# Kernel tuning notes

Hardware: AMD Instinct MI355X
Metric: run time of the kernel (lower is better)

Reference implementation:

```python
import jax, jax.numpy as jnp
import numpy as np

J_THR = 0.5
E_THR = 0.5
STRIDE = 4.0
N_LAYERS = 3
NFEAT = 256
SCORER_HIDDEN = 128


def setup_inputs() -> dict:
    key = jax.random.key(0)
    ks = jax.random.split(key, 8)
    B, C, h, w = 4, NFEAT, 128, 128
    inp = {
        "j_logits": jax.random.normal(ks[0], (B, 1, h, w), dtype=jnp.float32),
        "offsets": jax.random.uniform(ks[1], (B, 2, h, w), dtype=jnp.float32),
        "node_feats_map": jax.random.normal(ks[2], (B, C, h, w), dtype=jnp.float32) * 0.1,
        "W_self": jax.random.normal(ks[3], (N_LAYERS, C, C), dtype=jnp.float32) / np.sqrt(C).astype(np.float32),
        "W_nbr": jax.random.normal(ks[4], (N_LAYERS, C, C), dtype=jnp.float32) / np.sqrt(C).astype(np.float32),
        "b_gnn": jnp.zeros((N_LAYERS, C), dtype=jnp.float32),
        "Ws1": jax.random.normal(ks[5], (2 * C, SCORER_HIDDEN), dtype=jnp.float32) / np.sqrt(2.0 * C).astype(np.float32),
        "bs1": jnp.zeros((SCORER_HIDDEN,), dtype=jnp.float32),
        "Ws2": jax.random.normal(ks[6], (SCORER_HIDDEN,), dtype=jnp.float32) / np.sqrt(SCORER_HIDDEN).astype(np.float32),
        "bs2": jnp.zeros((), dtype=jnp.float32),
        "max_nodes": 256,
    }
    return inp


def _complete_graph(n):
    # src repeats node i (n-1) times; dst enumerates all j != i, matching torch complete_graph
    src = np.repeat(np.arange(n), n - 1)
    grid = np.tile(np.arange(n), (n, 1))
    dst = grid[~np.eye(n, dtype=bool)]
    return jnp.asarray(src, dtype=jnp.int32), jnp.asarray(dst, dtype=jnp.int32)


def reference(j_logits, offsets, node_feats_map, W_self, W_nbr, b_gnn, Ws1, bs1, Ws2, bs2, max_nodes):
    B, _, h, w = j_logits.shape
    C = node_feats_map.shape[1]
    N = int(max_nodes)
    src, dst = _complete_graph(N)  # [E], E = N*(N-1)

    def per_image(jl, off, nmap):
        prob = jax.nn.sigmoid(jl[0].reshape(-1))            # [h*w]
        topv, topi = jax.lax.top_k(prob, N)                  # fixed-size stream compaction
        valid = topv > J_THR                                 # [N] mask replacing dynamic nonzero
        iy = topi // w
        ix = topi % w
        yo = off[0].reshape(-1)[topi]
        xo = off[1].reshape(-1)[topi]
        xs = (ix.astype(jnp.float32) + 0.5 + xo) * STRIDE
        ys = (iy.astype(jnp.float32) + 0.5 + yo) * STRIDE
        nodes = jnp.stack([xs, ys], axis=-1)                 # [N,2]
        x = nmap.reshape(C, -1)[:, topi].T * valid[:, None].astype(nmap.dtype)  # [N,C]
        ev = (valid[src] & valid[dst]).astype(x.dtype)       # [E] edge validity
        deg = jax.ops.segment_sum(ev, dst, num_segments=N)   # [N]
        inv_deg = jnp.where(deg > 0, 1.0 / jnp.maximum(deg, 1.0), 0.0)
        for l in range(W_self.shape[0]):
            msg = x[src] * ev[:, None]                       # gather + mask [E,C]
            agg = jax.ops.segment_sum(msg, dst, num_segments=N) * inv_deg[:, None]
            x = jax.nn.relu(x @ W_self[l] + agg @ W_nbr[l] + b_gnn[l]) * valid[:, None].astype(x.dtype)
        hcat = jnp.concatenate([x[src], x[dst]], axis=-1)    # [E,2C]
        hid = jax.nn.relu(hcat @ Ws1 + bs1)                  # [E,H]
        logits = hid @ Ws2 + bs2                             # [E]
        probs = jax.nn.sigmoid(logits)
        keep = (probs > E_THR) & (ev > 0)
        return nodes, x, logits, keep

    nodes, node_emb, edge_logits, keep = jax.vmap(per_image)(j_logits, offsets, node_feats_map)
    return nodes, node_emb, edge_logits, keep
```

## Files before the change

kernel.cpp:

```cpp
#include <hip/hip_runtime.h>

#define NPIX 16384
#define NN   256
#define CC   256
#define HH   128
#define EE   65280
#define BB   4
#define NG   16

typedef __attribute__((ext_vector_type(8))) short short8;
typedef __attribute__((ext_vector_type(4))) float f32x4;

__device__ __forceinline__ unsigned short f2bf(float f){
  unsigned b = __float_as_uint(f);
  return (unsigned short)((b + 0x7fffu + ((b >> 16) & 1u)) >> 16);
}
__device__ __forceinline__ float bf2f(unsigned short s){ return __uint_as_float(((unsigned)s) << 16); }

__global__ __launch_bounds__(1024) void k_topk(
    const float* __restrict__ jl, const float* __restrict__ off,
    int* __restrict__ topi, int* __restrict__ valid, float* __restrict__ inv_deg,
    float* __restrict__ out_nodes, float* __restrict__ Sbuf,
    const float* __restrict__ Wself, const float* __restrict__ Wnbr,
    const float* __restrict__ Ws1,
    unsigned short* __restrict__ wbfT, unsigned short* __restrict__ wuvT)
{
  __shared__ int hist[NG][257];
  __shared__ int histT[256];
  __shared__ unsigned long long s_sel[NN];
  __shared__ unsigned long long s_T;
  __shared__ int s_digit, s_krem, s_cnt, s_vcnt, s_break;
  __shared__ float tile[32][33];

  const int bid = blockIdx.x;
  const int tid = threadIdx.x;

  if (bid >= BB) {
    const int blk = bid - BB;
    const int m = blk >> 6;
    const int t = blk & 63;
    const int r  = tid >> 5;
    const int cl = tid & 31;
    if (m < 6) {
      const int tr = t >> 3, tc = t & 7;
      const float* src = (m < 3) ? (Wself + (size_t)m*65536) : (Wnbr + (size_t)(m-3)*65536);
      tile[r][cl] = src[(size_t)(tr*32 + r)*256 + tc*32 + cl];
      __syncthreads();
      wbfT[(size_t)m*65536 + (size_t)(tc*32 + r)*256 + tr*32 + cl] = f2bf(tile[cl][r]);
    } else {
      const int tr = t >> 2, tc = t & 3;
      tile[r][cl] = Ws1[(size_t)(tr*32 + r)*128 + tc*32 + cl];
      __syncthreads();
      int h  = tc*32 + r;
      int cgx = tr*32 + cl;
      int col = h + ((cgx >= 256) ? 128 : 0);
      wuvT[(size_t)col*256 + (cgx & 255)] = f2bf(tile[cl][r]);
    }
    return;
  }

  const int b = bid;
  const int grp = tid >> 6;
  if (tid == 0) { s_cnt = 0; s_vcnt = 0; }

  {
    int l = tid >> 8, c = tid & 255;
    Sbuf[l*BB*CC + b*CC + c] = 0.0f;
  }

  unsigned long long rk[16];
  const float* p = jl + (size_t)b * NPIX;
  #pragma unroll
  for (int r = 0; r < 16; ++r) {
    int i = tid + (r << 10);
    float x = p[i];
    float pr = 1.0f / (1.0f + expf(-x));
    unsigned bits = __float_as_uint(pr);
    rk[r] = ((unsigned long long)bits << 32) | (unsigned)(0xFFFFFFFFu - (unsigned)i);
  }

  unsigned long long prefix = 0;
  int k = NN;
  int shift = 56;
  int brk = 0;
  for (int pass = 0; pass < 8 && !brk; ++pass) {
    shift = 56 - 8 * pass;
    for (int i = tid; i < NG * 257; i += 1024) ((int*)hist)[i] = 0;
    __syncthreads();
    unsigned long long pmask = (pass == 0) ? 0ULL : (~0ULL << (shift + 8));
    #pragma unroll
    for (int r = 0; r < 16; ++r) {
      unsigned long long kk = rk[r];
      if ((kk & pmask) == prefix)
        atomicAdd(&hist[grp][(int)((kk >> shift) & 255)], 1);
    }
    __syncthreads();
    if (tid < 256) {
      int t = 0;
      #pragma unroll
      for (int g = 0; g < NG; ++g) t += hist[g][tid];
      histT[tid] = t;
    }
    __syncthreads();
    if (tid < 64) {
      int h0 = histT[4*tid + 0], h1 = histT[4*tid + 1];
      int h2 = histT[4*tid + 2], h3 = histT[4*tid + 3];
      int tot = h0 + h1 + h2 + h3;
      int suf = tot;
      #pragma unroll
      for (int d = 1; d < 64; d <<= 1) {
        int o = __shfl_down(suf, d);
        if (tid + d < 64) suf += o;
      }
      int above = suf - tot;
      int c3 = h3 + above;
      int c2 = c3 + h2;
      int c1 = c2 + h1;
      int c0 = c1 + h0;
      if      (c3 >= k && above < k) { s_digit = 4*tid+3; s_krem = k - above; s_break = (h3 == 1); }
      else if (c2 >= k && c3    < k) { s_digit = 4*tid+2; s_krem = k - c3;    s_break = (h2 == 1); }
      else if (c1 >= k && c2    < k) { s_digit = 4*tid+1; s_krem = k - c2;    s_break = (h1 == 1); }
      else if (c0 >= k && c1    < k) { s_digit = 4*tid+0; s_krem = k - c1;    s_break = (h0 == 1); }
    }
    __syncthreads();
    prefix |= ((unsigned long long)s_digit) << shift;
    k = s_krem;
    brk = s_break;
  }

  if (shift == 0) {
    if (tid == 0) s_T = prefix;
  } else {
    unsigned long long known_mask = ~0ULL << shift;
    #pragma unroll
    for (int r = 0; r < 16; ++r)
      if ((rk[r] & known_mask) == prefix) s_T = rk[r];
  }
  __syncthreads();
  unsigned long long T = s_T;

  #pragma unroll
  for (int r = 0; r < 16; ++r) {
    unsigned long long kk = rk[r];
    if (kk >= T) { int pos = atomicAdd(&s_cnt, 1); s_sel[pos] = kk; }
  }
  __syncthreads();

  int my_rank = -1, my_v = 0;
  if (tid < NN) {
    unsigned long long mine = s_sel[tid];
    int rank = 0;
    #pragma unroll 16
    for (int j = 0; j < NN; ++j) rank += (s_sel[j] > mine) ? 1 : 0;
    unsigned bits = (unsigned)(mine >> 32);
    int v = bits > 0x3F000000u ? 1 : 0;
    int idx = (int)(0xFFFFFFFFu - (unsigned)(mine & 0xFFFFFFFFull));
    if (v) atomicAdd(&s_vcnt, 1);
    topi[b*NN + rank] = idx;
    valid[b*NN + rank] = v;
    int iy = idx >> 7;
    int ix = idx & 127;
    float yo = off[((size_t)b*2 + 0) * NPIX + idx];
    float xo = off[((size_t)b*2 + 1) * NPIX + idx];
    out_nodes[(b*NN + rank)*2 + 0] = ((float)ix + 0.5f + xo) * 4.0f;
    out_nodes[(b*NN + rank)*2 + 1] = ((float)iy + 0.5f + yo) * 4.0f;
    my_rank = rank; my_v = v;
  }
  __syncthreads();
  if (tid < NN) {
    int V = s_vcnt;
    inv_deg[b*NN + my_rank] = (my_v && V >= 2) ? 1.0f / (float)(V - 1) : 0.0f;
  }
}

__global__ __launch_bounds__(256) void k_gather(
    const float* __restrict__ nmap, const int* __restrict__ topi,
    const int* __restrict__ valid, unsigned short* __restrict__ x, float* __restrict__ S0)
{
  const int bn = blockIdx.x;
  const int b = bn >> 8;
  const int c = threadIdx.x;
  int pix = topi[bn];
  int v = valid[bn];
  float val = v ? nmap[(((size_t)b*CC + c) << 14) + pix] : 0.0f;
  unsigned short hb = f2bf(val);
  x[(size_t)bn*CC + c] = hb;
  float valr = bf2f(hb);
  if (valr != 0.0f) atomicAdd(&S0[b*CC + c], valr);
}

__global__ __launch_bounds__(256) void k_gnn(
    const unsigned short* __restrict__ x, const float* __restrict__ S,
    const float* __restrict__ inv_deg, const int* __restrict__ valid,
    const unsigned short* __restrict__ wT1, const unsigned short* __restrict__ wT2,
    const float* __restrict__ bias, unsigned short* __restrict__ xout,
    float* __restrict__ Snext,
    float* __restrict__ out_emb)
{
  __shared__ float sA1[16][33];
  __shared__ float sA2[16][33];
  __shared__ float sP2p[8][33];
  __shared__ float sP2[32];
  const int mt = blockIdx.x >> 3;
  const int cg = blockIdx.x & 7;
  const int row0 = mt * 16;
  const int b = row0 >> 8;
  const int tid = threadIdx.x;
  const int wave = tid >> 6;
  const int lane = tid & 63;

  {
    const int cl = tid >> 3;
    const int kw = tid & 7;
    const unsigned short* wrow = wT2 + (size_t)(cg*32 + cl)*256 + kw*32;
    const float* Sb = S + b*CC + kw*32;
    float a = 0.f;
    #pragma unroll 8
    for (int i = 0; i < 32; ++i) a += Sb[i] * bf2f(wrow[i]);
    sP2p[kw][cl] = a;
  }
  __syncthreads();
  if (tid < 32) {
    float s = 0.f;
    #pragma unroll
    for (int g = 0; g < 8; ++g) s += sP2p[g][tid];
    sP2[tid] = s;
  }

  const unsigned short* wT = (wave < 2) ? wT1 : wT2;
  const int colbase = cg*32 + (wave & 1)*16;
  const int arow = row0 + (lane & 15);
  const int koff = (lane >> 4) * 8;

  const short8* aptr = (const short8*)(x + (size_t)arow*256 + koff);
  const short8* bptr = (const short8*)(wT + (size_t)(colbase + (lane & 15))*256 + koff);

  f32x4 acc = {0.f, 0.f, 0.f, 0.f};
  #pragma unroll
  for (int kk = 0; kk < 8; ++kk) {
    short8 af = aptr[kk*4];
    short8 bf = bptr[kk*4];
    acc = __builtin_amdgcn_mfma_f32_16x16x32_bf16(af, bf, acc, 0, 0, 0);
  }

  {
    float* dst = (wave < 2) ? &sA1[0][0] : &sA2[0][0];
    int ccol = (wave & 1)*16 + (lane & 15);
    #pragma unroll
    for (int r = 0; r < 4; ++r) {
      int crow = (lane >> 4)*4 + r;
      dst[crow*33 + ccol] = acc[r];
    }
  }
  __syncthreads();

  const int row = tid >> 4;
  const int cp2 = tid & 15;
  const int gr = row0 + row;
  const int c0 = cg*32 + 2*cp2;
  float inv = inv_deg[gr];
  int   va  = valid[gr];
  float a10 = sA1[row][2*cp2], a11 = sA1[row][2*cp2+1];
  float a20 = sA2[row][2*cp2], a21 = sA2[row][2*cp2+1];
  float p0 = sP2[2*cp2], p1 = sP2[2*cp2+1];
  float o0 = fmaxf(a10 + inv*(p0 - a20) + bias[c0],     0.f); o0 = va ? o0 : 0.f;
  float o1 = fmaxf(a11 + inv*(p1 - a21) + bias[c0 + 1], 0.f); o1 = va ? o1 : 0.f;

  unsigned short h0 = f2bf(o0), h1 = f2bf(o1);
  ((unsigned*)xout)[(size_t)gr*128 + (cg*16 + cp2)] = (unsigned)h0 | ((unsigned)h1 << 16);
  if (out_emb) {
    float2 v; v.x = o0; v.y = o1;
    *(float2*)&out_emb[(size_t)gr*CC + c0] = v;
  }
  if (Snext) {
    __syncthreads();
    sA1[row][2*cp2]   = bf2f(h0);
    sA1[row][2*cp2+1] = bf2f(h1);
    __syncthreads();
    if (tid < 32) {
      float s = 0.f;
      #pragma unroll
      for (int r = 0; r < 16; ++r) s += sA1[r][tid];
      if (s != 0.f) atomicAdd(&Snext[b*CC + cg*32 + tid], s);
    }
  }
}

__global__ __launch_bounds__(256) void k_uv(
    const unsigned short* __restrict__ x, const unsigned short* __restrict__ wuvT,
    const float* __restrict__ bs1,
    float* __restrict__ u, float* __restrict__ vt)
{
  const int mt = blockIdx.x >> 2;
  const int cg = blockIdx.x & 3;
  const int row0 = mt * 16;
  const int b = row0 >> 8;
  const int wave = threadIdx.x >> 6;
  const int lane = threadIdx.x & 63;
  const int col = cg*64 + wave*16 + (lane & 15);
  const int arow = row0 + (lane & 15);
  const int koff = (lane >> 4) * 8;
  const short8* aptr = (const short8*)(x + (size_t)arow*256 + koff);
  const short8* bptr = (const short8*)(wuvT + (size_t)col*256 + koff);
  f32x4 acc = {0.f, 0.f, 0.f, 0.f};
  #pragma unroll
  for (int kk = 0; kk < 8; ++kk)
    acc = __builtin_amdgcn_mfma_f32_16x16x32_bf16(aptr[kk*4], bptr[kk*4], acc, 0, 0, 0);
  const int rbase = row0 + (lane >> 4)*4;
  if (col < HH) {
    float bv = bs1[col];
    #pragma unroll
    for (int r = 0; r < 4; ++r)
      u[(size_t)(rbase + r)*HH + col] = acc[r] + bv;
  } else {
    float4 v; v.x = acc[0]; v.y = acc[1]; v.z = acc[2]; v.w = acc[3];
    *(float4*)&vt[(size_t)(b*HH + (col - HH))*NN + rbase] = v;
  }
}

__global__ __launch_bounds__(256) void k_edges(
    const float* __restrict__ u, const float* __restrict__ vt,
    const float* __restrict__ Ws2, const float* __restrict__ bs2,
    const int* __restrict__ valid,
    float* __restrict__ out_logits, float* __restrict__ out_keep)
{
  __shared__ float su[4][HH];
  __shared__ float sws[HH];
  __shared__ float4 red[3][4][64];
  const int b  = blockIdx.x >> 6;
  const int ig = blockIdx.x & 63;
  const int i0 = ig * 4;
  const int tid = threadIdx.x;
  const int jq = tid & 63;
  const int kh = tid >> 6;

  #pragma unroll
  for (int r = 0; r < 2; ++r) {
    int idx = tid + 256*r;
    int il = idx >> 7, h = idx & 127;
    su[il][h] = u[((size_t)(b*NN + i0 + il))*HH + h];
  }
  if (tid < HH) sws[tid] = Ws2[tid];
  __syncthreads();

  const float4* vbase = (const float4*)(vt + (size_t)(b*HH + kh*32)*NN) + jq;
  float4 acc0 = {0,0,0,0}, acc1 = {0,0,0,0}, acc2 = {0,0,0,0}, acc3 = {0,0,0,0};
  #pragma unroll 4
  for (int h = 0; h < 32; ++h) {
    float4 v = vbase[(size_t)h*64];
    float wh = sws[kh*32 + h];
    float u0 = su[0][kh*32 + h];
    float u1 = su[1][kh*32 + h];
    float u2 = su[2][kh*32 + h];
    float u3 = su[3][kh*32 + h];
    acc0.x += fmaxf(u0 + v.x, 0.f)*wh; acc0.y += fmaxf(u0 + v.y, 0.f)*wh;
    acc0.z += fmaxf(u0 + v.z, 0.f)*wh; acc0.w += fmaxf(u0 + v.w, 0.f)*wh;
    acc1.x += fmaxf(u1 + v.x, 0.f)*wh; acc1.y += fmaxf(u1 + v.y, 0.f)*wh;
    acc1.z += fmaxf(u1 + v.z, 0.f)*wh; acc1.w += fmaxf(u1 + v.w, 0.f)*wh;
    acc2.x += fmaxf(u2 + v.x, 0.f)*wh; acc2.y += fmaxf(u2 + v.y, 0.f)*wh;
    acc2.z += fmaxf(u2 + v.z, 0.f)*wh; acc2.w += fmaxf(u2 + v.w, 0.f)*wh;
    acc3.x += fmaxf(u3 + v.x, 0.f)*wh; acc3.y += fmaxf(u3 + v.y, 0.f)*wh;
    acc3.z += fmaxf(u3 + v.z, 0.f)*wh; acc3.w += fmaxf(u3 + v.w, 0.f)*wh;
  }
  if (kh > 0) {
    red[kh-1][0][jq] = acc0;
    red[kh-1][1][jq] = acc1;
    red[kh-1][2][jq] = acc2;
    red[kh-1][3][jq] = acc3;
  }
  __syncthreads();
  if (kh == 0) {
    float bs = bs2[0];
    float* Lb = out_logits + (size_t)b*EE;
    float* Kb = out_keep   + (size_t)b*EE;
    int j0 = 4*jq;
    int vj0 = valid[b*NN + j0 + 0];
    int vj1 = valid[b*NN + j0 + 1];
    int vj2 = valid[b*NN + j0 + 2];
    int vj3 = valid[b*NN + j0 + 3];
    #pragma unroll
    for (int il = 0; il < 4; ++il) {
      int i = i0 + il;
      int vi = valid[b*NN + i];
      float4 a = (il == 0) ? acc0 : (il == 1) ? acc1 : (il == 2) ? acc2 : acc3;
      float4 r0 = red[0][il][jq], r1 = red[1][il][jq], r2 = red[2][il][jq];
      float lg0 = a.x + r0.x + r1.x + r2.x + bs;
      float lg1 = a.y + r0.y + r1.y + r2.y + bs;
      float lg2 = a.z + r0.z + r1.z + r2.z + bs;
      float lg3 = a.w + r0.w + r1.w + r2.w + bs;
      {
        int j = j0;
        if (j != i) { int e = i*255 + (j < i ? j : j-1);
          Lb[e] = lg0; Kb[e] = (lg0 > 0.f && vi && vj0) ? 1.0f : 0.0f; }
      }
      {
        int j = j0 + 1;
        if (j != i) { int e = i*255 + (j < i ? j : j-1);
          Lb[e] = lg1; Kb[e] = (lg1 > 0.f && vi && vj1) ? 1.0f : 0.0f; }
      }
      {
        int j = j0 + 2;
        if (j != i) { int e = i*255 + (j < i ? j : j-1);
          Lb[e] = lg2; Kb[e] = (lg2 > 0.f && vi && vj2) ? 1.0f : 0.0f; }
      }
      {
        int j = j0 + 3;
        if (j != i) { int e = i*255 + (j < i ? j : j-1);
          Lb[e] = lg3; Kb[e] = (lg3 > 0.f && vi && vj3) ? 1.0f : 0.0f; }
      }
    }
  }
}

extern "C" void kernel_launch(void* const* d_in, const int* in_sizes, int n_in,
                              void* d_out, int out_size, void* d_ws, size_t ws_size,
                              hipStream_t stream) {
  const float* jl    = (const float*)d_in[0];
  const float* off   = (const float*)d_in[1];
  const float* nmap  = (const float*)d_in[2];
  const float* Wself = (const float*)d_in[3];
  const float* Wnbr  = (const float*)d_in[4];
  const float* bg    = (const float*)d_in[5];
  const float* Ws1   = (const float*)d_in[6];
  const float* bs1   = (const float*)d_in[7];
  const float* Ws2   = (const float*)d_in[8];
  const float* bs2   = (const float*)d_in[9];

  char* ws = (char*)d_ws;
  int*   topi    = (int*)  (ws + 0);
  int*   valid   = (int*)  (ws + 4096);
  float* inv_deg = (float*)(ws + 8192);
  float* Sbuf    = (float*)(ws + 12288);
  unsigned short* xa = (unsigned short*)(ws + 28672);
  unsigned short* xb = (unsigned short*)(ws + 552960);
  float* u       = (float*)(ws + 1077248);
  float* vt      = (float*)(ws + 1601536);
  unsigned short* wbfT = (unsigned short*)(ws + 2125824);
  unsigned short* wuvT = (unsigned short*)(ws + 2912256);

  float* out        = (float*)d_out;
  float* out_nodes  = out;
  float* out_emb    = out + 2048;
  float* out_logits = out + 264192;
  float* out_keep   = out + 525312;

  hipLaunchKernelGGL(k_topk,   dim3(BB + 448), dim3(1024), 0, stream,
                     jl, off, topi, valid, inv_deg, out_nodes, Sbuf,
                     Wself, Wnbr, Ws1, wbfT, wuvT);
  hipLaunchKernelGGL(k_gather, dim3(BB*NN),    dim3(256),  0, stream,
                     nmap, topi, valid, xa, Sbuf);

  unsigned short* xc = xa; unsigned short* xn = xb;
  for (int l = 0; l < 3; ++l) {
    hipLaunchKernelGGL(k_gnn, dim3(512), dim3(256),  0, stream,
                       xc, Sbuf + l*BB*CC, inv_deg, valid,
                       wbfT + (size_t)l*65536, wbfT + (size_t)(3 + l)*65536, bg + l*CC,
                       xn,
                       (l < 2) ? (Sbuf + (l+1)*BB*CC) : (float*)nullptr,
                       (l == 2) ? out_emb : (float*)nullptr);
    unsigned short* t = xc; xc = xn; xn = t;
  }

  hipLaunchKernelGGL(k_uv,    dim3(256),   dim3(256), 0, stream, xc, wuvT, bs1, u, vt);
  hipLaunchKernelGGL(k_edges, dim3(BB*64), dim3(256), 0, stream,
                     u, vt, Ws2, bs2, valid, out_logits, out_keep);
}
```

Baseline: 76.91 us.

## Batch gather rows per block, vectorize S·W dot, widen top-k histogram groups

Three unrelated tweaks land together. The gather kernel now handles 8 nodes per block and accumulates the column sum locally, which cuts atomics to S0 by eightfold and shrinks the launch to 128 blocks. The k_gnn prologue dot product now reads weights as uint4 and S as float4, unpacking bf16 pairs in place of scalar loads. The top-k histogram uses 32 groups of 32 threads instead of 16 groups of 64, which should lower shared-atomic contention but doubles histogram shared memory and the merge work.

```diff
diff --git a/kernel.cpp b/kernel.cpp
--- a/kernel.cpp
+++ b/kernel.cpp
@@ -6,7 +6,7 @@
 #define HH   128
 #define EE   65280
 #define BB   4
-#define NG   16
+#define NG   32
 
 typedef __attribute__((ext_vector_type(8))) short short8;
 typedef __attribute__((ext_vector_type(4))) float f32x4;
@@ -16,6 +16,8 @@
   return (unsigned short)((b + 0x7fffu + ((b >> 16) & 1u)) >> 16);
 }
 __device__ __forceinline__ float bf2f(unsigned short s){ return __uint_as_float(((unsigned)s) << 16); }
+__device__ __forceinline__ float bf_lo(unsigned u){ return __uint_as_float(u << 16); }
+__device__ __forceinline__ float bf_hi(unsigned u){ return __uint_as_float(u & 0xFFFF0000u); }
 
 __global__ __launch_bounds__(1024) void k_topk(
     const float* __restrict__ jl, const float* __restrict__ off,
@@ -60,7 +62,7 @@
   }
 
   const int b = bid;
-  const int grp = tid >> 6;
+  const int grp = tid >> 5;
   if (tid == 0) { s_cnt = 0; s_vcnt = 0; }
 
   {
@@ -177,16 +179,23 @@
     const float* __restrict__ nmap, const int* __restrict__ topi,
     const int* __restrict__ valid, unsigned short* __restrict__ x, float* __restrict__ S0)
 {
-  const int bn = blockIdx.x;
-  const int b = bn >> 8;
+  __shared__ int s_pix[8], s_val[8];
+  const int blk = blockIdx.x;
+  const int b  = blk >> 5;
+  const int n0 = (blk & 31) * 8;
   const int c = threadIdx.x;
-  int pix = topi[bn];
-  int v = valid[bn];
-  float val = v ? nmap[(((size_t)b*CC + c) << 14) + pix] : 0.0f;
-  unsigned short hb = f2bf(val);
-  x[(size_t)bn*CC + c] = hb;
-  float valr = bf2f(hb);
-  if (valr != 0.0f) atomicAdd(&S0[b*CC + c], valr);
+  if (c < 8) { s_pix[c] = topi[b*NN + n0 + c]; s_val[c] = valid[b*NN + n0 + c]; }
+  __syncthreads();
+  const float* base = nmap + ((size_t)b*CC + c) * NPIX;
+  float sum = 0.f;
+  #pragma unroll
+  for (int r = 0; r < 8; ++r) {
+    float val = s_val[r] ? base[s_pix[r]] : 0.0f;
+    unsigned short hb = f2bf(val);
+    x[(size_t)(b*NN + n0 + r)*CC + c] = hb;
+    sum += bf2f(hb);
+  }
+  if (sum != 0.0f) atomicAdd(&S0[b*CC + c], sum);
 }
 
 __global__ __launch_bounds__(256) void k_gnn(
@@ -212,11 +221,16 @@
   {
     const int cl = tid >> 3;
     const int kw = tid & 7;
-    const unsigned short* wrow = wT2 + (size_t)(cg*32 + cl)*256 + kw*32;
-    const float* Sb = S + b*CC + kw*32;
+    const uint4*  w4 = (const uint4*)(wT2 + (size_t)(cg*32 + cl)*256 + kw*32);
+    const float4* S4 = (const float4*)(S + b*CC + kw*32);
     float a = 0.f;
-    #pragma unroll 8
-    for (int i = 0; i < 32; ++i) a += Sb[i] * bf2f(wrow[i]);
+    #pragma unroll
+    for (int i = 0; i < 4; ++i) {
+      uint4 q = w4[i];
+      float4 s0 = S4[2*i], s1 = S4[2*i + 1];
+      a += s0.x*bf_lo(q.x) + s0.y*bf_hi(q.x) + s0.z*bf_lo(q.y) + s0.w*bf_hi(q.y);
+      a += s1.x*bf_lo(q.z) + s1.y*bf_hi(q.z) + s1.z*bf_lo(q.w) + s1.w*bf_hi(q.w);
+    }
     sP2p[kw][cl] = a;
   }
   __syncthreads();
@@ -447,7 +461,7 @@
   hipLaunchKernelGGL(k_topk,   dim3(BB + 448), dim3(1024), 0, stream,
                      jl, off, topi, valid, inv_deg, out_nodes, Sbuf,
                      Wself, Wnbr, Ws1, wbfT, wuvT);
-  hipLaunchKernelGGL(k_gather, dim3(BB*NN),    dim3(256),  0, stream,
+  hipLaunchKernelGGL(k_gather, dim3(BB*32),    dim3(256),  0, stream,
                      nmap, topi, valid, xa, Sbuf);
 
   unsigned short* xc = xa; unsigned short* xn = xb;
```

Result: faster. 72.43 us, median of 2 (-5.8%).
